# Optimization experiments

Measured on AMD Instinct MI355X. Metric: run time of the kernel, lower is better.

The kernel has to match this reference:

```python
import jax, jax.numpy as jnp
import numpy as np

N = 6144
ATT_DIM = 128
HID = int(ATT_DIM * 0.75)  # 96
EDGE_EMB_DIM = 20
N_EDGE_TYPES = 3
E_PER_TYPE = 100000
NUM_LAYERS = 2
NUM_HEADS = 2
NEG_SLOPE = 0.2


def _leaky(x):
    return jnp.where(x > 0, x, NEG_SLOPE * x)


def setup_inputs() -> dict:
    key = jax.random.key(0)
    ks = jax.random.split(key, 8)
    inputs = jax.random.normal(ks[0], (N, ATT_DIM), dtype=jnp.float32)
    edges = jax.random.randint(ks[1], (N_EDGE_TYPES, 2, E_PER_TYPE), 0, N, dtype=jnp.int64)
    # ScoringNetwork params (Linear stored as [in, out])
    W1 = jax.random.normal(ks[2], (ATT_DIM, HID), dtype=jnp.float32) * (1.0 / np.sqrt(ATT_DIM))
    b1 = jnp.zeros((HID,), dtype=jnp.float32)
    W2 = jax.random.normal(ks[3], (HID, 1), dtype=jnp.float32) * (1.0 / np.sqrt(HID))
    b2 = jnp.zeros((1,), dtype=jnp.float32)
    # shared edge-type embeddings
    edge_emb = jax.random.normal(ks[4], (N_EDGE_TYPES, EDGE_EMB_DIM), dtype=jnp.float32) * 0.1
    # per-layer, per-head attention weights [L, H, edge_emb_dim+2, 1]
    attn_w = jax.random.normal(ks[5], (NUM_LAYERS, NUM_HEADS, EDGE_EMB_DIM + 2, 1), dtype=jnp.float32) * 0.1
    return {"inputs": inputs, "edges": edges, "W1": W1, "b1": b1,
            "W2": W2, "b2": b2, "edge_emb": edge_emb, "attn_w": attn_w}


def reference(inputs, edges, W1, b1, W2, b2, edge_emb, attn_w):
    n = inputs.shape[0]
    T, _, E = edges.shape
    src = edges[:, 0, :].reshape(-1)  # [T*E]
    tgt = edges[:, 1, :].reshape(-1)  # [T*E]
    # ScoringNetwork: linear2(leakyrelu(linear1(x)))  -> [N, 1]
    scores = _leaky(inputs @ W1 + b1) @ W2 + b2
    L, H = attn_w.shape[0], attn_w.shape[1]
    for l in range(L):
        acc = jnp.zeros_like(scores)
        s = scores[:, 0]  # [N]
        for h in range(H):
            w = attn_w[l, h, :, 0]  # [edge_emb_dim + 2]
            # concat([src_score, edge_emb, tgt_score]) @ w, computed factored
            emb_score = edge_emb @ w[1:-1]  # [T]
            e = w[0] * s[src] + jnp.repeat(emb_score, E) + w[-1] * s[tgt]  # [T*E]
            # scatter-add into dense NxN (accumulates across edge types)
            A = jnp.zeros((n, n), dtype=scores.dtype).at[src, tgt].add(e)
            att = jax.nn.softmax(_leaky(A), axis=-1)  # dense row softmax (incl. non-edges)
            acc = acc + att @ scores
        scores = acc / H
    return scores
```

## Files before the change

### kernel.cpp

```cpp
#include <hip/hip_runtime.h>

#define N_NODES 6144
#define ATTD 128
#define HIDD 96
#define EPT 100000
#define NTYPE 3
#define NEDGE (NTYPE * EPT)
#define SUBS 4
#define SUBCAP 48
#define RSTRIDE (SUBS * SUBCAP)
#define CSTRIDE 16
#define MCAP 128
#define PSTRIDE 16
#define NCELL 64
#define NEG 0.2f
#define BUCKET_BLOCKS ((NEDGE + 255) / 256)
#define MLP_BLOCKS (N_NODES / 2)

__global__ void k_build(const int* __restrict__ edges, int* __restrict__ rcnt,
                        int* __restrict__ bucket,
                        const float* __restrict__ X, const float* __restrict__ W1,
                        const float* __restrict__ b1, const float* __restrict__ W2,
                        const float* __restrict__ b2, float* __restrict__ s,
                        float* __restrict__ part0) {
    int bid = blockIdx.x;
    if (bid < BUCKET_BLOCKS) {
        int k = bid * 256 + threadIdx.x;
        if (k < NEDGE) {
            int t = k / EPT;
            int e = k - t * EPT;
            int src = edges[t * (2 * EPT) + e];
            int tgt = edges[t * (2 * EPT) + EPT + e];
            int sub = k & (SUBS - 1);
            int pos = atomicAdd(&rcnt[(src * SUBS + sub) * CSTRIDE], 1);
            if (pos < SUBCAP) bucket[src * RSTRIDE + sub * SUBCAP + pos] = (t << 13) | tgt;
        }
        return;
    }
    int half = threadIdx.x >> 7;
    int tid  = threadIdx.x & 127;
    int mbid = bid - BUCKET_BLOCKS;
    int row  = mbid * 2 + half;
    __shared__ float xs[2][ATTD];
    __shared__ float red[2][2];
    __shared__ float sred[2];
    xs[half][tid] = X[row * ATTD + tid];
    __syncthreads();
    float val = 0.f;
    if (tid < HIDD) {
        float acc = b1[tid];
#pragma unroll 8
        for (int k = 0; k < ATTD; ++k) acc += xs[half][k] * W1[k * HIDD + tid];
        float h = acc > 0.f ? acc : NEG * acc;
        val = h * W2[tid];
    }
#pragma unroll
    for (int off = 32; off; off >>= 1) val += __shfl_down(val, off, 64);
    if ((threadIdx.x & 63) == 0) red[half][tid >> 6] = val;
    __syncthreads();
    if (tid == 0) {
        float r = red[half][0] + red[half][1] + b2[0];
        s[row] = r;
        sred[half] = r;
    }
    __syncthreads();
    if (threadIdx.x == 0)
        atomicAdd(&part0[(mbid & (NCELL - 1)) * PSTRIDE], sred[0] + sred[1]);
}

__global__ void k_gather1(const int* __restrict__ rcnt, const int* __restrict__ bucket,
                          const float* __restrict__ s,
                          const float* __restrict__ edge_emb,
                          const float* __restrict__ attn_w,
                          const float* __restrict__ part0, float* __restrict__ s2,
                          int2* __restrict__ mlist, int* __restrict__ cnt2,
                          float* __restrict__ part1) {
    int tid = threadIdx.x, lane = tid & 63, wv = tid >> 6, bid = blockIdx.x;
    __shared__ int hk[4 * 256];
    __shared__ int hc[4 * 256];
    __shared__ float pl[32];
    __shared__ float stot_s;
    __shared__ float wsum[4];
    if (tid < 4) {
        const float* w = attn_w + tid * 22;
        float* p = pl + tid * 8;
        p[0] = w[0];
        p[1] = w[21];
        for (int ty = 0; ty < NTYPE; ++ty) {
            float acc = 0.f;
            for (int j = 0; j < 20; ++j) acc += edge_emb[ty * 20 + j] * w[1 + j];
            p[2 + ty] = acc;
        }
    }
    int* K = hk + wv * 256;
    int* C = hc + wv * 256;
#pragma unroll
    for (int j = lane; j < 256; j += 64) { K[j] = -1; C[j] = 0; }
    if (wv == 0) {
        float v = part0[lane * PSTRIDE];
#pragma unroll
        for (int off = 32; off; off >>= 1) v += __shfl_down(v, off, 64);
        if (lane == 0) stot_s = v;
    }
    __syncthreads();
    const int u = bid * 4 + wv;
    for (int sdx = 0; sdx < SUBS; ++sdx) {
        int d = rcnt[(u * SUBS + sdx) * CSTRIDE];
        if (d > SUBCAP) d = SUBCAP;
        for (int i = lane; i < d; i += 64) {
            int raw = bucket[u * RSTRIDE + sdx * SUBCAP + i];
            int v = raw & 8191;
            int t = raw >> 13;
            unsigned slot = ((unsigned)v * 2654435761u) >> 24;
            while (true) {
                int prev = atomicCAS(&K[slot], -1, v);
                if (prev == -1 || prev == v) break;
                slot = (slot + 1) & 255;
            }
            atomicAdd(&C[slot], 1 << (10 * t));
        }
    }
    __syncthreads();
    float su = s[u];
    float w00 = pl[0], w01 = pl[1], e00 = pl[2], e01 = pl[3], e02 = pl[4];
    float w10 = pl[8], w11 = pl[9], e10 = pl[10], e11 = pl[11], e12 = pl[12];
    float num0 = 0.f, den0 = 0.f, num1 = 0.f, den1 = 0.f;
    int base = 0;
#pragma unroll
    for (int it = 0; it < 4; ++it) {
        int j = it * 64 + lane;
        int key = K[j];
        bool live = key >= 0;
        unsigned long long m = __ballot(live);
        if (live) {
            int cw = C[j];
            int idx = base + __popcll(m & ((1ull << lane) - 1ull));
            mlist[u * MCAP + idx] = make_int2(key, cw);
            float c0 = (float)(cw & 1023);
            float c1 = (float)((cw >> 10) & 1023);
            float c2 = (float)((cw >> 20) & 1023);
            float Cc = c0 + c1 + c2;
            float sv = s[key];
            float A0 = Cc * (w00 * su + w01 * sv) + c0 * e00 + c1 * e01 + c2 * e02;
            float la0 = A0 > 0.f ? A0 : NEG * A0;
            float g0 = expf(la0) - 1.f;
            num0 += g0 * sv; den0 += g0;
            float A1 = Cc * (w10 * su + w11 * sv) + c0 * e10 + c1 * e11 + c2 * e12;
            float la1 = A1 > 0.f ? A1 : NEG * A1;
            float g1 = expf(la1) - 1.f;
            num1 += g1 * sv; den1 += g1;
        }
        base += __popcll(m);
    }
#pragma unroll
    for (int off = 32; off; off >>= 1) {
        num0 += __shfl_down(num0, off, 64);
        den0 += __shfl_down(den0, off, 64);
        num1 += __shfl_down(num1, off, 64);
        den1 += __shfl_down(den1, off, 64);
    }
    if (lane == 0) {
        cnt2[u] = base;
        float S = stot_s;
        float r0 = (S + num0) / ((float)N_NODES + den0);
        float r1 = (S + num1) / ((float)N_NODES + den1);
        float val = 0.5f * (r0 + r1);
        s2[u] = val;
        wsum[wv] = val;
    }
    __syncthreads();
    if (tid == 0)
        atomicAdd(&part1[(bid & (NCELL - 1)) * PSTRIDE],
                  wsum[0] + wsum[1] + wsum[2] + wsum[3]);
}

__global__ void k_gather2(const int* __restrict__ cnt2, const int2* __restrict__ mlist,
                          const float* __restrict__ s,
                          const float* __restrict__ edge_emb,
                          const float* __restrict__ attn_w,
                          const float* __restrict__ part1, float* __restrict__ dst) {
    int tid = threadIdx.x, lane = tid & 63, wv = tid >> 6, bid = blockIdx.x;
    __shared__ float pl[32];
    __shared__ float stot_s;
    if (tid < 4) {
        const float* w = attn_w + tid * 22;
        float* p = pl + tid * 8;
        p[0] = w[0];
        p[1] = w[21];
        for (int ty = 0; ty < NTYPE; ++ty) {
            float acc = 0.f;
            for (int j = 0; j < 20; ++j) acc += edge_emb[ty * 20 + j] * w[1 + j];
            p[2 + ty] = acc;
        }
    }
    if (wv == 0) {
        float v = part1[lane * PSTRIDE];
#pragma unroll
        for (int off = 32; off; off >>= 1) v += __shfl_down(v, off, 64);
        if (lane == 0) stot_s = v;
    }
    __syncthreads();
    const int u = bid * 4 + wv;
    float su = s[u];
    float w00 = pl[16], w01 = pl[17], e00 = pl[18], e01 = pl[19], e02 = pl[20];
    float w10 = pl[24], w11 = pl[25], e10 = pl[26], e11 = pl[27], e12 = pl[28];
    float num0 = 0.f, den0 = 0.f, num1 = 0.f, den1 = 0.f;
    int d = cnt2[u];
    for (int i = lane; i < d; i += 64) {
        int2 vc = mlist[u * MCAP + i];
        int v  = vc.x;
        int cw = vc.y;
        float c0 = (float)(cw & 1023);
        float c1 = (float)((cw >> 10) & 1023);
        float c2 = (float)((cw >> 20) & 1023);
        float Cc = c0 + c1 + c2;
        float sv = s[v];
        float A0 = Cc * (w00 * su + w01 * sv) + c0 * e00 + c1 * e01 + c2 * e02;
        float la0 = A0 > 0.f ? A0 : NEG * A0;
        float g0 = expf(la0) - 1.f;
        num0 += g0 * sv; den0 += g0;
        float A1 = Cc * (w10 * su + w11 * sv) + c0 * e10 + c1 * e11 + c2 * e12;
        float la1 = A1 > 0.f ? A1 : NEG * A1;
        float g1 = expf(la1) - 1.f;
        num1 += g1 * sv; den1 += g1;
    }
#pragma unroll
    for (int off = 32; off; off >>= 1) {
        num0 += __shfl_down(num0, off, 64);
        den0 += __shfl_down(den0, off, 64);
        num1 += __shfl_down(num1, off, 64);
        den1 += __shfl_down(den1, off, 64);
    }
    if (lane == 0) {
        float S = stot_s;
        float r0 = (S + num0) / ((float)N_NODES + den0);
        float r1 = (S + num1) / ((float)N_NODES + den1);
        dst[u] = 0.5f * (r0 + r1);
    }
}

extern "C" void kernel_launch(void* const* d_in, const int* in_sizes, int n_in,
                              void* d_out, int out_size, void* d_ws, size_t ws_size,
                              hipStream_t stream) {
    const float* X        = (const float*)d_in[0];
    const int*   edges    = (const int*)d_in[1];
    const float* W1       = (const float*)d_in[2];
    const float* b1       = (const float*)d_in[3];
    const float* W2       = (const float*)d_in[4];
    const float* b2       = (const float*)d_in[5];
    const float* edge_emb = (const float*)d_in[6];
    const float* attn_w   = (const float*)d_in[7];
    float* out = (float*)d_out;

    char* w = (char*)d_ws;
    float* part0  = (float*)w; w += NCELL * PSTRIDE * sizeof(float);
    float* part1  = (float*)w; w += NCELL * PSTRIDE * sizeof(float);
    int*   rcnt   = (int*)w;   w += N_NODES * SUBS * CSTRIDE * sizeof(int);
    size_t zbytes = (size_t)(w - (char*)d_ws);
    float* s      = (float*)w; w += N_NODES * sizeof(float);
    float* s2     = (float*)w; w += N_NODES * sizeof(float);
    int*   cnt2   = (int*)w;   w += N_NODES * sizeof(int);
    int*   bucket = (int*)w;   w += N_NODES * RSTRIDE * sizeof(int);
    int2*  mlist  = (int2*)w;

    hipMemsetAsync(d_ws, 0, zbytes, stream);
    k_build<<<BUCKET_BLOCKS + MLP_BLOCKS, 256, 0, stream>>>(edges, rcnt, bucket,
                                                            X, W1, b1, W2, b2, s, part0);
    k_gather1<<<N_NODES / 4, 256, 0, stream>>>(rcnt, bucket, s, edge_emb, attn_w,
                                               part0, s2, mlist, cnt2, part1);
    k_gather2<<<N_NODES / 4, 256, 0, stream>>>(cnt2, mlist, s2, edge_emb, attn_w,
                                               part1, out);
}
```

Before: 54.48 us.

## Compact edge buckets to 16-bit, pack match list into one int, halve MLP blocks

Replaces the four sub-buckets per source node with a single 128-entry bucket that stores each (type, target) pair as a 16-bit value. The counter memset and the bucket traffic both shrink. The merged neighbour list now packs the node id and three 6-bit type counts into one 32-bit word instead of an int2, halving gather2's reads. Each MLP block processes four rows over two passes, halving the number of blocks. The trade-off is that all edges from a source now contend on one atomic counter, and counts above 63 per type would overflow the packed field.

```diff
diff --git a/kernel.cpp b/kernel.cpp
--- a/kernel.cpp
+++ b/kernel.cpp
@@ -6,19 +6,16 @@
 #define EPT 100000
 #define NTYPE 3
 #define NEDGE (NTYPE * EPT)
-#define SUBS 4
-#define SUBCAP 48
-#define RSTRIDE (SUBS * SUBCAP)
-#define CSTRIDE 16
-#define MCAP 128
+#define BCAP 128
+#define CPAD 16
 #define PSTRIDE 16
 #define NCELL 64
 #define NEG 0.2f
 #define BUCKET_BLOCKS ((NEDGE + 255) / 256)
-#define MLP_BLOCKS (N_NODES / 2)
+#define MLP_BLOCKS (N_NODES / 4)
 
 __global__ void k_build(const int* __restrict__ edges, int* __restrict__ rcnt,
-                        int* __restrict__ bucket,
+                        unsigned short* __restrict__ bucket,
                         const float* __restrict__ X, const float* __restrict__ W1,
                         const float* __restrict__ b1, const float* __restrict__ W2,
                         const float* __restrict__ b2, float* __restrict__ s,
@@ -31,49 +28,55 @@
             int e = k - t * EPT;
             int src = edges[t * (2 * EPT) + e];
             int tgt = edges[t * (2 * EPT) + EPT + e];
-            int sub = k & (SUBS - 1);
-            int pos = atomicAdd(&rcnt[(src * SUBS + sub) * CSTRIDE], 1);
-            if (pos < SUBCAP) bucket[src * RSTRIDE + sub * SUBCAP + pos] = (t << 13) | tgt;
+            int pos = atomicAdd(&rcnt[src * CPAD], 1);
+            if (pos < BCAP)
+                bucket[src * BCAP + pos] = (unsigned short)((t << 13) | tgt);
         }
         return;
     }
-    int half = threadIdx.x >> 7;
-    int tid  = threadIdx.x & 127;
     int mbid = bid - BUCKET_BLOCKS;
-    int row  = mbid * 2 + half;
+    const int half = threadIdx.x >> 7;
+    const int t128 = threadIdx.x & 127;
     __shared__ float xs[2][ATTD];
     __shared__ float red[2][2];
     __shared__ float sred[2];
-    xs[half][tid] = X[row * ATTD + tid];
-    __syncthreads();
-    float val = 0.f;
-    if (tid < HIDD) {
-        float acc = b1[tid];
+    float blocksum = 0.f;
+    for (int pass = 0; pass < 2; ++pass) {
+        int row = (mbid << 2) + (pass << 1) + half;
+        __syncthreads();
+        xs[half][t128] = X[row * ATTD + t128];
+        __syncthreads();
+        float val = 0.f;
+        if (t128 < HIDD) {
+            float acc = b1[t128];
 #pragma unroll 8
-        for (int k = 0; k < ATTD; ++k) acc += xs[half][k] * W1[k * HIDD + tid];
-        float h = acc > 0.f ? acc : NEG * acc;
-        val = h * W2[tid];
-    }
-#pragma unroll
-    for (int off = 32; off; off >>= 1) val += __shfl_down(val, off, 64);
-    if ((threadIdx.x & 63) == 0) red[half][tid >> 6] = val;
-    __syncthreads();
-    if (tid == 0) {
-        float r = red[half][0] + red[half][1] + b2[0];
-        s[row] = r;
-        sred[half] = r;
-    }
-    __syncthreads();
+            for (int k = 0; k < ATTD; ++k) acc += xs[half][k] * W1[k * HIDD + t128];
+            float h = acc > 0.f ? acc : NEG * acc;
+            val = h * W2[t128];
+        }
+#pragma unroll
+        for (int off = 32; off; off >>= 1) val += __shfl_down(val, off, 64);
+        if ((threadIdx.x & 63) == 0) red[half][t128 >> 6] = val;
+        __syncthreads();
+        if (t128 == 0) {
+            float r = red[half][0] + red[half][1] + b2[0];
+            s[row] = r;
+            sred[half] = r;
+        }
+        __syncthreads();
+        if (threadIdx.x == 0) blocksum += sred[0] + sred[1];
+    }
     if (threadIdx.x == 0)
-        atomicAdd(&part0[(mbid & (NCELL - 1)) * PSTRIDE], sred[0] + sred[1]);
-}
-
-__global__ void k_gather1(const int* __restrict__ rcnt, const int* __restrict__ bucket,
+        atomicAdd(&part0[(mbid & (NCELL - 1)) * PSTRIDE], blocksum);
+}
+
+__global__ void k_gather1(const int* __restrict__ rcnt,
+                          const unsigned short* __restrict__ bucket,
                           const float* __restrict__ s,
                           const float* __restrict__ edge_emb,
                           const float* __restrict__ attn_w,
                           const float* __restrict__ part0, float* __restrict__ s2,
-                          int2* __restrict__ mlist, int* __restrict__ cnt2,
+                          int* __restrict__ mlist, int* __restrict__ cnt2,
                           float* __restrict__ part1) {
     int tid = threadIdx.x, lane = tid & 63, wv = tid >> 6, bid = blockIdx.x;
     __shared__ int hk[4 * 256];
@@ -104,11 +107,11 @@
     }
     __syncthreads();
     const int u = bid * 4 + wv;
-    for (int sdx = 0; sdx < SUBS; ++sdx) {
-        int d = rcnt[(u * SUBS + sdx) * CSTRIDE];
-        if (d > SUBCAP) d = SUBCAP;
+    {
+        int d = rcnt[u * CPAD];
+        if (d > BCAP) d = BCAP;
         for (int i = lane; i < d; i += 64) {
-            int raw = bucket[u * RSTRIDE + sdx * SUBCAP + i];
+            int raw = bucket[u * BCAP + i];
             int v = raw & 8191;
             int t = raw >> 13;
             unsigned slot = ((unsigned)v * 2654435761u) >> 24;
@@ -134,11 +137,10 @@
         unsigned long long m = __ballot(live);
         if (live) {
             int cw = C[j];
+            int ic0 = cw & 1023, ic1 = (cw >> 10) & 1023, ic2 = (cw >> 20) & 1023;
             int idx = base + __popcll(m & ((1ull << lane) - 1ull));
-            mlist[u * MCAP + idx] = make_int2(key, cw);
-            float c0 = (float)(cw & 1023);
-            float c1 = (float)((cw >> 10) & 1023);
-            float c2 = (float)((cw >> 20) & 1023);
+            mlist[u * BCAP + idx] = key | (ic0 << 13) | (ic1 << 19) | (ic2 << 25);
+            float c0 = (float)ic0, c1 = (float)ic1, c2 = (float)ic2;
             float Cc = c0 + c1 + c2;
             float sv = s[key];
             float A0 = Cc * (w00 * su + w01 * sv) + c0 * e00 + c1 * e01 + c2 * e02;
@@ -174,7 +176,7 @@
                   wsum[0] + wsum[1] + wsum[2] + wsum[3]);
 }
 
-__global__ void k_gather2(const int* __restrict__ cnt2, const int2* __restrict__ mlist,
+__global__ void k_gather2(const int* __restrict__ cnt2, const int* __restrict__ mlist,
                           const float* __restrict__ s,
                           const float* __restrict__ edge_emb,
                           const float* __restrict__ attn_w,
@@ -207,12 +209,11 @@
     float num0 = 0.f, den0 = 0.f, num1 = 0.f, den1 = 0.f;
     int d = cnt2[u];
     for (int i = lane; i < d; i += 64) {
-        int2 vc = mlist[u * MCAP + i];
-        int v  = vc.x;
-        int cw = vc.y;
-        float c0 = (float)(cw & 1023);
-        float c1 = (float)((cw >> 10) & 1023);
-        float c2 = (float)((cw >> 20) & 1023);
+        int p = mlist[u * BCAP + i];
+        int v = p & 8191;
+        float c0 = (float)((p >> 13) & 63);
+        float c1 = (float)((p >> 19) & 63);
+        float c2 = (float)((p >> 25) & 63);
         float Cc = c0 + c1 + c2;
         float sv = s[v];
         float A0 = Cc * (w00 * su + w01 * sv) + c0 * e00 + c1 * e01 + c2 * e02;
@@ -255,13 +256,13 @@
     char* w = (char*)d_ws;
     float* part0  = (float*)w; w += NCELL * PSTRIDE * sizeof(float);
     float* part1  = (float*)w; w += NCELL * PSTRIDE * sizeof(float);
-    int*   rcnt   = (int*)w;   w += N_NODES * SUBS * CSTRIDE * sizeof(int);
+    int*   rcnt   = (int*)w;   w += N_NODES * CPAD * sizeof(int);
     size_t zbytes = (size_t)(w - (char*)d_ws);
     float* s      = (float*)w; w += N_NODES * sizeof(float);
     float* s2     = (float*)w; w += N_NODES * sizeof(float);
     int*   cnt2   = (int*)w;   w += N_NODES * sizeof(int);
-    int*   bucket = (int*)w;   w += N_NODES * RSTRIDE * sizeof(int);
-    int2*  mlist  = (int2*)w;
+    int*   mlist  = (int*)w;   w += N_NODES * BCAP * sizeof(int);
+    unsigned short* bucket = (unsigned short*)w;
 
     hipMemsetAsync(d_ws, 0, zbytes, stream);
     k_build<<<BUCKET_BLOCKS + MLP_BLOCKS, 256, 0, stream>>>(edges, rcnt, bucket,
```

Measured after the change: 53.54 us. No clear change (-1.7%).
